# Performance work log

Measured on AMD Instinct MI355X. Metric: run time of the kernel, lower is better.

The kernel has to match this reference:

```python
import jax, jax.numpy as jnp
import numpy as np

HIDDEN = 2048
HEADS = 16
HEAD_DIM = HIDDEN // HEADS


def setup_inputs() -> dict:
    key = jax.random.key(0)
    k1, k2, k3, k4, k5 = jax.random.split(key, 5)
    scale = 1.0 / np.sqrt(HIDDEN)
    x = jax.random.normal(k1, (2, 2048, HIDDEN), dtype=jnp.float32)
    # nn.Linear weights stored as [out_features, in_features]
    w_q = jax.random.normal(k2, (HIDDEN, HIDDEN), dtype=jnp.float32) * scale
    w_k = jax.random.normal(k3, (HEAD_DIM, HIDDEN), dtype=jnp.float32) * scale
    w_v = jax.random.normal(k4, (HEAD_DIM, HIDDEN), dtype=jnp.float32) * scale
    w_out = jax.random.normal(k5, (HIDDEN, HIDDEN), dtype=jnp.float32) * scale
    return {"x": x, "w_q": w_q, "w_k": w_k, "w_v": w_v, "w_out": w_out}


def reference(x, w_q, w_k, w_v, w_out) -> jnp.ndarray:
    bsz, seq_len, _ = x.shape
    norm = jnp.asarray(np.sqrt(HEAD_DIM), dtype=x.dtype)
    # projections (Linear: x @ W^T)
    q = (x @ w_q.T).reshape(bsz, seq_len, HEADS, HEAD_DIM)  # [b,s,h,d]
    k = x @ w_k.T  # [b,s,d] single shared KV head
    v = x @ w_v.T  # [b,s,d]
    # attention scores: [b,h,s,s], K/V broadcast across heads
    att = jnp.einsum("bshd,btd->bhst", q, k) / norm
    att = jax.nn.softmax(att, axis=-1)
    out = jnp.einsum("bhst,btd->bshd", att, v).reshape(bsz, seq_len, HIDDEN)
    return out @ w_out.T
```

## Files before the change

### kernel.cpp

```cpp
#include <hip/hip_runtime.h>


using bf16   = __bf16;
using bf16x2 = __bf16 __attribute__((ext_vector_type(2)));
using bf16x4 = __bf16 __attribute__((ext_vector_type(4)));
using bf16x8 = __bf16 __attribute__((ext_vector_type(8)));
using f32x4  = float  __attribute__((ext_vector_type(4)));
using u32x4  = unsigned __attribute__((ext_vector_type(4)));

#define GAS __attribute__((address_space(1)))
#define LAS __attribute__((address_space(3)))

__device__ __forceinline__ void load_lds16(const bf16* g, bf16* l) {
    __builtin_amdgcn_global_load_lds((const GAS void*)g, (LAS void*)l, 16, 0, 0);
}

__device__ __forceinline__ unsigned pkbf(float a, float b) {
    bf16x2 t; t[0] = (bf16)a; t[1] = (bf16)b;
    return __builtin_bit_cast(unsigned, t);
}
__device__ __forceinline__ void perm32(unsigned& a, unsigned& b) {
    asm volatile("v_permlane32_swap_b32 %0, %1" : "+v"(a), "+v"(b));
}
__device__ __forceinline__ void perm16(unsigned& a, unsigned& b) {
    asm volatile("v_permlane16_swap_b32 %0, %1" : "+v"(a), "+v"(b));
}

#define Q_SCALE_LOG2 0.12751745f

__global__ __launch_bounds__(256) void cvt_all(
    const float* __restrict__ x,  const float* __restrict__ wq,
    const float* __restrict__ wk, const float* __restrict__ wv,
    const float* __restrict__ wo, bf16* __restrict__ dst)
{
    const size_t i = (size_t)(blockIdx.x * 256 + threadIdx.x) * 8;
    const float* src; size_t off;
    if      (i <  8388608) { src = x;  off = 0; }
    else if (i < 12582912) { src = wq; off = 8388608; }
    else if (i < 12845056) { src = wk; off = 12582912; }
    else if (i < 13107200) { src = wv; off = 12845056; }
    else                   { src = wo; off = 13107200; }
    float4 f0 = *(const float4*)(src + (i - off));
    float4 f1 = *(const float4*)(src + (i - off) + 4);
    bf16x8 v;
    v[0] = (bf16)f0.x; v[1] = (bf16)f0.y; v[2] = (bf16)f0.z; v[3] = (bf16)f0.w;
    v[4] = (bf16)f1.x; v[5] = (bf16)f1.y; v[6] = (bf16)f1.z; v[7] = (bf16)f1.w;
    *(bf16x8*)(dst + i) = v;
}

__device__ __forceinline__ void gemm128(
    const bf16* __restrict__ A, const bf16* __restrict__ B, void* __restrict__ Cp,
    int bm, int bn, int ldC, int mode, float scale)
{
    __shared__ bf16 As[128 * 32];
    __shared__ bf16 Bs[128 * 32];
    const int K = 2048;

    const int tid  = threadIdx.x;
    const int wave = tid >> 6;
    const int lane = tid & 63;
    const int quad = lane >> 4;
    const int c    = lane & 15;
    const int wm   = (wave >> 1) << 6;
    const int wn   = (wave & 1) << 6;

    const int srow = tid >> 2;
    const int scol = (tid & 3) << 3;
    const bf16* Ag = A + (size_t)(bm + srow) * K + scol;
    const bf16* Bg = B + (size_t)(bn + srow) * K + scol;
    bf16* lA = As + wave * 512;
    bf16* lB = Bs + wave * 512;

    f32x4 acc[4][4];
#pragma unroll
    for (int i = 0; i < 4; ++i)
#pragma unroll
        for (int j = 0; j < 4; ++j)
            acc[i][j] = f32x4{0.f, 0.f, 0.f, 0.f};

    for (int k0 = 0; k0 < K; k0 += 32) {
        load_lds16(Ag + k0,          lA);
        load_lds16(Ag + k0 + 64 * K, lA + 2048);
        load_lds16(Bg + k0,          lB);
        load_lds16(Bg + k0 + 64 * K, lB + 2048);
        __syncthreads();

        bf16x8 af[4], bfv[4];
#pragma unroll
        for (int i = 0; i < 4; ++i)
            af[i] = *(const bf16x8*)(As + (wm + i * 16 + c) * 32 + quad * 8);
#pragma unroll
        for (int j = 0; j < 4; ++j)
            bfv[j] = *(const bf16x8*)(Bs + (wn + j * 16 + c) * 32 + quad * 8);
#pragma unroll
        for (int i = 0; i < 4; ++i)
#pragma unroll
            for (int j = 0; j < 4; ++j)
                acc[i][j] = __builtin_amdgcn_mfma_f32_16x16x32_bf16(af[i], bfv[j], acc[i][j], 0, 0, 0);
        __syncthreads();
    }

    if (mode == 0) {
        bf16* C = (bf16*)Cp;
#pragma unroll
        for (int i = 0; i < 4; ++i) {
            const int m = bm + wm + i * 16 + quad * 4;
#pragma unroll
            for (int j = 0; j < 4; ++j) {
                const int n = bn + wn + j * 16 + c;
#pragma unroll
                for (int r = 0; r < 4; ++r)
                    C[(size_t)(m + r) * ldC + n] = (bf16)(acc[i][j][r] * scale);
            }
        }
    } else if (mode == 1) {
        bf16* C = (bf16*)Cp;
#pragma unroll
        for (int j = 0; j < 4; ++j) {
            const int n = bn + wn + j * 16 + c;
#pragma unroll
            for (int i = 0; i < 4; ++i) {
                const int m = bm + wm + i * 16 + quad * 4;
                bf16x4 v;
#pragma unroll
                for (int r = 0; r < 4; ++r) v[r] = (bf16)acc[i][j][r];
                *(bf16x4*)(C + (size_t)n * ldC + m) = v;
            }
        }
    } else {
        float* C = (float*)Cp;
#pragma unroll
        for (int i = 0; i < 4; ++i) {
            const int m = bm + wm + i * 16 + quad * 4;
#pragma unroll
            for (int j = 0; j < 4; ++j) {
                const int n = bn + wn + j * 16 + c;
#pragma unroll
                for (int r = 0; r < 4; ++r)
                    C[(size_t)(m + r) * ldC + n] = acc[i][j][r];
            }
        }
    }
}

__global__ __launch_bounds__(256, 3) void qkv_kernel(
    const bf16* __restrict__ x,  const bf16* __restrict__ wq,
    const bf16* __restrict__ wk, const bf16* __restrict__ wv,
    bf16* __restrict__ Qb, bf16* __restrict__ Kb, bf16* __restrict__ Vt)
{
    const int bx = blockIdx.x;
    const int bm = blockIdx.y << 7;
    const bf16* B; bf16* C; int ldC, bn, mode; float sc;
    if (bx < 16)       { B = wq; C = Qb; ldC = 2048; bn = bx << 7; mode = 0; sc = Q_SCALE_LOG2; }
    else if (bx == 16) { B = wk; C = Kb; ldC = 128;  bn = 0;       mode = 0; sc = 1.0f; }
    else               { B = wv; C = Vt; ldC = 4096; bn = 0;       mode = 1; sc = 1.0f; }
    gemm128(x, B, C, bm, bn, ldC, mode, sc);
}

__global__ __launch_bounds__(256, 3) void out_kernel(
    const bf16* __restrict__ AO, const bf16* __restrict__ wo, float* __restrict__ out)
{
    gemm128(AO, wo, out, blockIdx.y << 7, blockIdx.x << 7, 2048, 2, 1.0f);
}

#define KS_LD 136
#define VS_LD 72

__global__ __launch_bounds__(256, 2) void attn_kernel(
    const bf16* __restrict__ Qb, const bf16* __restrict__ Kb,
    const bf16* __restrict__ Vt, bf16* __restrict__ P0,
    bf16* __restrict__ P1, float* __restrict__ Lp)
{
    __shared__ bf16 Ks[64 * KS_LD];
    __shared__ bf16 Vs[128 * VS_LD];

    const int tid  = threadIdx.x;
    const int lane = tid & 63;
    const int wave = tid >> 6;
    const int q    = lane >> 4;
    const int c    = lane & 15;
    const int qt = blockIdx.x, h = blockIdx.y;
    const int b = blockIdx.z & 1, chunk = blockIdx.z >> 1;
    const int tbeg = chunk << 10;
    const int rowbase = b * 2048 + qt * 128;
    const int wrow = wave * 32;
    bf16* Pout = chunk ? P1 : P0;

    bf16x8 qf[2][4];
#pragma unroll
    for (int nq = 0; nq < 2; ++nq)
#pragma unroll
        for (int ks = 0; ks < 4; ++ks)
            qf[nq][ks] = *(const bf16x8*)(Qb + (size_t)(rowbase + wrow + nq * 16 + c) * 2048
                                             + h * 128 + ks * 32 + q * 8);

    f32x4 o[8][2];
#pragma unroll
    for (int mtv = 0; mtv < 8; ++mtv)
#pragma unroll
        for (int nq = 0; nq < 2; ++nq) o[mtv][nq] = f32x4{0.f, 0.f, 0.f, 0.f};

    float psum[2] = {0.f, 0.f};

    const int krow = tid >> 4, kcol = (tid & 15) << 3;
    const int vrow = tid >> 3, vcol = (tid & 7) << 3;
    const bf16* Kg = Kb + (size_t)b * 2048 * 128;
    const bf16* Vg = Vt + (size_t)b * 2048;

    for (int t0 = tbeg; t0 < tbeg + 1024; t0 += 64) {
        bf16x8 kreg[4], vreg[4];
#pragma unroll
        for (int p = 0; p < 4; ++p)
            kreg[p] = *(const bf16x8*)(Kg + (size_t)(t0 + p * 16 + krow) * 128 + kcol);
#pragma unroll
        for (int p = 0; p < 4; ++p)
            vreg[p] = *(const bf16x8*)(Vg + (size_t)(p * 32 + vrow) * 4096 + t0 + vcol);

        __syncthreads();
#pragma unroll
        for (int p = 0; p < 4; ++p)
            *(bf16x8*)(Ks + (p * 16 + krow) * KS_LD + kcol) = kreg[p];
#pragma unroll
        for (int p = 0; p < 4; ++p)
            *(bf16x8*)(Vs + (p * 32 + vrow) * VS_LD + vcol) = vreg[p];
        __syncthreads();

        f32x4 s[4][2];
#pragma unroll
        for (int mt = 0; mt < 4; ++mt)
#pragma unroll
            for (int nq = 0; nq < 2; ++nq) s[mt][nq] = f32x4{0.f, 0.f, 0.f, 0.f};
#pragma unroll
        for (int ks = 0; ks < 4; ++ks) {
            bf16x8 kf[4];
#pragma unroll
            for (int mt = 0; mt < 4; ++mt)
                kf[mt] = *(const bf16x8*)(Ks + (mt * 16 + c) * KS_LD + ks * 32 + q * 8);
#pragma unroll
            for (int mt = 0; mt < 4; ++mt)
#pragma unroll
                for (int nq = 0; nq < 2; ++nq)
                    s[mt][nq] = __builtin_amdgcn_mfma_f32_16x16x32_bf16(kf[mt], qf[nq][ks], s[mt][nq], 0, 0, 0);
        }

#pragma unroll
        for (int j = 0; j < 2; ++j) {
            bf16x8 vb[8];
#pragma unroll
            for (int mtv = 0; mtv < 8; ++mtv)
                vb[mtv] = *(const bf16x8*)(Vs + (mtv * 16 + c) * VS_LD + j * 32 + q * 8);
#pragma unroll
            for (int nq = 0; nq < 2; ++nq) {
                const float e0 = __builtin_amdgcn_exp2f(s[2 * j][nq][0]);
                const float e1 = __builtin_amdgcn_exp2f(s[2 * j][nq][1]);
                const float e2 = __builtin_amdgcn_exp2f(s[2 * j][nq][2]);
                const float e3 = __builtin_amdgcn_exp2f(s[2 * j][nq][3]);
                const float e4 = __builtin_amdgcn_exp2f(s[2 * j + 1][nq][0]);
                const float e5 = __builtin_amdgcn_exp2f(s[2 * j + 1][nq][1]);
                const float e6 = __builtin_amdgcn_exp2f(s[2 * j + 1][nq][2]);
                const float e7 = __builtin_amdgcn_exp2f(s[2 * j + 1][nq][3]);
                psum[nq] += ((e0 + e1) + (e2 + e3)) + ((e4 + e5) + (e6 + e7));
                unsigned a0 = pkbf(e0, e1);
                unsigned a1 = pkbf(e2, e3);
                unsigned b0 = pkbf(e4, e5);
                unsigned b1 = pkbf(e6, e7);
                perm32(a0, b0); perm32(a1, b1);
                perm16(a0, b0); perm16(a1, b1);
                const bf16x8 pf = __builtin_bit_cast(bf16x8, u32x4{a0, a1, b0, b1});
#pragma unroll
                for (int mtv = 0; mtv < 8; ++mtv)
                    o[mtv][nq] = __builtin_amdgcn_mfma_f32_16x16x32_bf16(vb[mtv], pf, o[mtv][nq], 0, 0, 0);
            }
        }
    }

#pragma unroll
    for (int nq = 0; nq < 2; ++nq) {
        float v = psum[nq];
        v += __shfl_xor(v, 16);
        v += __shfl_xor(v, 32);
        psum[nq] = v;
    }

#pragma unroll
    for (int nq = 0; nq < 2; ++nq) {
        const float rinv = 1.0f / psum[nq];
        const size_t row = (size_t)(rowbase + wrow + nq * 16 + c) * 2048 + h * 128;
#pragma unroll
        for (int mtv = 0; mtv < 8; ++mtv) {
            bf16x4 v;
#pragma unroll
            for (int r = 0; r < 4; ++r) v[r] = (bf16)(o[mtv][nq][r] * rinv);
            *(bf16x4*)(Pout + row + mtv * 16 + q * 4) = v;
        }
        if (q == 0)
            Lp[((size_t)((chunk * 2 + b) * 16 + h)) * 2048 + qt * 128 + wrow + nq * 16 + c] = psum[nq];
    }
}

__global__ __launch_bounds__(256) void merge_kernel(
    const bf16* __restrict__ P0, const bf16* __restrict__ P1,
    const float* __restrict__ Lp, bf16* __restrict__ AO)
{
    const int row = blockIdx.x;
    const int t = threadIdx.x;
    const int h = t >> 4;
    const int b = row >> 11, qrow = row & 2047;
    const float l1 = Lp[(size_t)(b * 16 + h) * 2048 + qrow];
    const float l2 = Lp[(size_t)((2 + b) * 16 + h) * 2048 + qrow];
    const float w1 = l1 / (l1 + l2);
    const float w2 = 1.0f - w1;
    const size_t off = (size_t)row * 2048 + t * 8;
    const bf16x8 a = *(const bf16x8*)(P0 + off);
    const bf16x8 bb = *(const bf16x8*)(P1 + off);
    bf16x8 ov;
#pragma unroll
    for (int r = 0; r < 8; ++r)
        ov[r] = (bf16)((float)a[r] * w1 + (float)bb[r] * w2);
    *(bf16x8*)(AO + off) = ov;
}

extern "C" void kernel_launch(void* const* d_in, const int* in_sizes, int n_in,
                              void* d_out, int out_size, void* d_ws, size_t ws_size,
                              hipStream_t stream)
{
    const float* x  = (const float*)d_in[0];
    const float* wq = (const float*)d_in[1];
    const float* wk = (const float*)d_in[2];
    const float* wv = (const float*)d_in[3];
    const float* wo = (const float*)d_in[4];
    float* out = (float*)d_out;

    char* ws = (char*)d_ws;
    const size_t MB = 1024 * 1024;
    bf16* xb  = (bf16*)(ws);
    bf16* wqb = (bf16*)(ws + 16 * MB);
    bf16* wkb = (bf16*)(ws + 24 * MB);
    bf16* wvb = (bf16*)(ws + 24 * MB + 512 * 1024);
    bf16* wob = (bf16*)(ws + 25 * MB);
    bf16* Qb  = (bf16*)(ws + 33 * MB);
    bf16* AO  = Qb;
    bf16* Kb  = (bf16*)(ws + 49 * MB);
    bf16* Vt  = (bf16*)(ws + 50 * MB);
    bf16* P0  = (bf16*)(ws);
    bf16* P1  = (bf16*)d_out;
    float* Lp = (float*)(ws + 16 * MB);

    cvt_all<<<17301504 / 2048, 256, 0, stream>>>(x, wq, wk, wv, wo, xb);
    qkv_kernel<<<dim3(18, 32), 256, 0, stream>>>(xb, wqb, wkb, wvb, Qb, Kb, Vt);
    attn_kernel<<<dim3(16, 16, 4), 256, 0, stream>>>(Qb, Kb, Vt, P0, P1, Lp);
    merge_kernel<<<4096, 256, 0, stream>>>(P0, P1, Lp, AO);
    out_kernel<<<dim3(16, 32), 256, 0, stream>>>(AO, wob, out);
}
```

Measured before the change: 293.9 us.

## Load attention K/V tiles directly to LDS with XOR swizzle

Replaces the register-staged global-to-LDS copy of K and V tiles with direct global_load_lds transfers. The padded LDS layouts become unpadded XOR-swizzled layouts so MFMA fragment reads stay bank-conflict free. This also frees LDS and registers, so occupancy is raised to 3 blocks per CU. The next tile's load is still issued after compute behind a barrier in a single buffer, so load latency is not overlapped with compute within a block. It relies on other resident blocks to hide that latency.

```diff
diff --git a/kernel.cpp b/kernel.cpp
--- a/kernel.cpp
+++ b/kernel.cpp
@@ -163,16 +163,13 @@
     gemm128(AO, wo, out, blockIdx.y << 7, blockIdx.x << 7, 2048, 2, 1.0f);
 }
 
-#define KS_LD 136
-#define VS_LD 72
-
-__global__ __launch_bounds__(256, 2) void attn_kernel(
+__global__ __launch_bounds__(256, 3) void attn_kernel(
     const bf16* __restrict__ Qb, const bf16* __restrict__ Kb,
     const bf16* __restrict__ Vt, bf16* __restrict__ P0,
     bf16* __restrict__ P1, float* __restrict__ Lp)
 {
-    __shared__ bf16 Ks[64 * KS_LD];
-    __shared__ bf16 Vs[128 * VS_LD];
+    __shared__ bf16 Ks[64 * 128];
+    __shared__ bf16 Vs[128 * 64];
 
     const int tid  = threadIdx.x;
     const int lane = tid & 63;
@@ -202,29 +199,30 @@
 
     float psum[2] = {0.f, 0.f};
 
-    const int krow = tid >> 4, kcol = (tid & 15) << 3;
-    const int vrow = tid >> 3, vcol = (tid & 7) << 3;
     const bf16* Kg = Kb + (size_t)b * 2048 * 128;
     const bf16* Vg = Vt + (size_t)b * 2048;
 
+    const int swkE = (((lane & 15) ^ (lane >> 4)) << 4);
+    const int swkO = swkE ^ 0x40;
+    const int swv  = (((lane & 7) ^ (lane >> 3)) << 4);
+    const int krow = (lane >> 4);
+    const int vrow = (lane >> 3);
+    const int c7s  = (c & 7) << 4;
+
+    {
+        const int t0 = tbeg;
+#pragma unroll
+        for (int p = 0; p < 4; ++p) {
+            const int i = wave * 4 + p;
+            load_lds16(Kg + (size_t)(t0 + i * 4 + krow) * 128 + (((p & 1) ? swkO : swkE) >> 1),
+                       Ks + i * 512);
+            load_lds16(Vg + (size_t)(i * 8 + vrow) * 4096 + t0 + (swv >> 1),
+                       Vs + i * 512);
+        }
+    }
+    __syncthreads();
+
     for (int t0 = tbeg; t0 < tbeg + 1024; t0 += 64) {
-        bf16x8 kreg[4], vreg[4];
-#pragma unroll
-        for (int p = 0; p < 4; ++p)
-            kreg[p] = *(const bf16x8*)(Kg + (size_t)(t0 + p * 16 + krow) * 128 + kcol);
-#pragma unroll
-        for (int p = 0; p < 4; ++p)
-            vreg[p] = *(const bf16x8*)(Vg + (size_t)(p * 32 + vrow) * 4096 + t0 + vcol);
-
-        __syncthreads();
-#pragma unroll
-        for (int p = 0; p < 4; ++p)
-            *(bf16x8*)(Ks + (p * 16 + krow) * KS_LD + kcol) = kreg[p];
-#pragma unroll
-        for (int p = 0; p < 4; ++p)
-            *(bf16x8*)(Vs + (p * 32 + vrow) * VS_LD + vcol) = vreg[p];
-        __syncthreads();
-
         f32x4 s[4][2];
 #pragma unroll
         for (int mt = 0; mt < 4; ++mt)
@@ -235,7 +233,8 @@
             bf16x8 kf[4];
 #pragma unroll
             for (int mt = 0; mt < 4; ++mt)
-                kf[mt] = *(const bf16x8*)(Ks + (mt * 16 + c) * KS_LD + ks * 32 + q * 8);
+                kf[mt] = *(const bf16x8*)((const char*)Ks
+                          + (mt * 16 + c) * 256 + ((ks * 64 + q * 16) ^ c7s));
 #pragma unroll
             for (int mt = 0; mt < 4; ++mt)
 #pragma unroll
@@ -248,7 +247,8 @@
             bf16x8 vb[8];
 #pragma unroll
             for (int mtv = 0; mtv < 8; ++mtv)
-                vb[mtv] = *(const bf16x8*)(Vs + (mtv * 16 + c) * VS_LD + j * 32 + q * 8);
+                vb[mtv] = *(const bf16x8*)((const char*)Vs
+                           + (mtv * 16 + c) * 128 + ((j * 64 + q * 16) ^ c7s));
 #pragma unroll
             for (int nq = 0; nq < 2; ++nq) {
                 const float e0 = __builtin_amdgcn_exp2f(s[2 * j][nq][0]);
@@ -272,6 +272,20 @@
                     o[mtv][nq] = __builtin_amdgcn_mfma_f32_16x16x32_bf16(vb[mtv], pf, o[mtv][nq], 0, 0, 0);
             }
         }
+
+        __syncthreads();
+        if (t0 + 64 < tbeg + 1024) {
+            const int tn = t0 + 64;
+#pragma unroll
+            for (int p = 0; p < 4; ++p) {
+                const int i = wave * 4 + p;
+                load_lds16(Kg + (size_t)(tn + i * 4 + krow) * 128 + (((p & 1) ? swkO : swkE) >> 1),
+                           Ks + i * 512);
+                load_lds16(Vg + (size_t)(i * 8 + vrow) * 4096 + tn + (swv >> 1),
+                           Vs + i * 512);
+            }
+            __syncthreads();
+        }
     }
 
 #pragma unroll
```

Result: slower. 463.7 us (+57.7%).
